# Optimization experiments

Hardware: AMD Instinct MI355X
Metric: run time of the kernel (lower is better)

Reference implementation:

```python
import jax, jax.numpy as jnp
import numpy as np

B, S, D, H = 2, 2048, 1024, 16
DK = D // H

def setup_inputs() -> dict:
    key = jax.random.key(0)
    ks = jax.random.split(key, 12)
    s = 1.0 / np.sqrt(D)
    inp = {
        'q': jax.random.normal(ks[0], (B, S, D), jnp.float32),
        'k': jax.random.normal(ks[1], (B, S, D), jnp.float32),
        'v': jax.random.normal(ks[2], (B, S, D), jnp.float32),
        'mask': jnp.tril(jnp.ones((S, S), jnp.int32))[None, None],  # [1,1,S,S] causal
        'Wq': jax.random.normal(ks[3], (D, D), jnp.float32) * s,
        'bq': jax.random.normal(ks[4], (D,), jnp.float32) * s,
        'Wk': jax.random.normal(ks[5], (D, D), jnp.float32) * s,
        'bk': jax.random.normal(ks[6], (D,), jnp.float32) * s,
        'Wv': jax.random.normal(ks[7], (D, D), jnp.float32) * s,
        'bv': jax.random.normal(ks[8], (D,), jnp.float32) * s,
        'Wo': jax.random.normal(ks[9], (D, D), jnp.float32) * s,
        'bo': jax.random.normal(ks[10], (D,), jnp.float32) * s,
    }
    return inp

def reference(q, k, v, mask, Wq, bq, Wk, bk, Wv, bv, Wo, bo):
    # linear projections (torch nn.Linear: x @ W.T + b)
    query = q @ Wq.T + bq
    key_ = k @ Wk.T + bk
    value = v @ Wv.T + bv
    # [B,S,D] -> [B,H,S,dk]
    def split_heads(x):
        return x.reshape(B, S, H, DK).transpose(0, 2, 1, 3)
    query, key_, value = split_heads(query), split_heads(key_), split_heads(value)
    scores = jnp.einsum('bhqd,bhkd->bhqk', query, key_) / jnp.sqrt(jnp.float32(DK))
    scores = jnp.where(mask == 0, jnp.float32(-1e9), scores)
    # FAITHFUL to source: softmax over dim=1 (the HEAD axis), not dim=-1
    attn = jax.nn.softmax(scores, axis=1)
    x = jnp.einsum('bhqk,bhkd->bhqd', attn, value)
    x = x.transpose(0, 2, 1, 3).reshape(B, S, D)
    return x @ Wo.T + bo
```

## Files before the change

kernel.cpp:

```cpp
#include <hip/hip_runtime.h>
#include <hip/hip_bf16.h>
#include <stdint.h>
#include <stddef.h>


typedef __attribute__((ext_vector_type(8))) __bf16 bf16x8;
typedef __attribute__((ext_vector_type(4))) __bf16 bf16x4;
typedef __attribute__((ext_vector_type(2))) _Float16 f16x2;
typedef __attribute__((ext_vector_type(4))) _Float16 f16x4;
typedef __attribute__((ext_vector_type(8))) _Float16 f16x8;
typedef __attribute__((ext_vector_type(4))) float  f32x4;
typedef __attribute__((ext_vector_type(8))) float  f32x8;

#define MFMA_BF16_K32(a,b,c) __builtin_amdgcn_mfma_f32_16x16x32_bf16((a),(b),(c),0,0,0)
#define MFMA_F16_K16(a,b,c)  __builtin_amdgcn_mfma_f32_16x16x16f16((a),(b),(c),0,0,0)

template <typename T> __device__ inline f32x8 ld8(const T* p);
template <> __device__ inline f32x8 ld8<float>(const float* p) { return *(const f32x8*)p; }
template <> __device__ inline f32x8 ld8<__bf16>(const __bf16* p) {
  return __builtin_convertvector(*(const bf16x8*)p, f32x8);
}

__device__ __forceinline__ void gl_lds16(const __bf16* g, __bf16* l) {
  __builtin_amdgcn_global_load_lds(
      (const __attribute__((address_space(1))) void*)g,
      (__attribute__((address_space(3))) void*)l, 16, 0, 0);
}

__device__ __forceinline__ f16x2 pk2(float a, float b) {
  return __builtin_bit_cast(f16x2, __builtin_amdgcn_cvt_pkrtz(a, b));
}

__device__ __forceinline__ void epi_store(int mode, float val, int m, int n, void* dst) {
  if (mode == 0) {
    ((float*)dst)[(size_t)m * 1024 + n] = val;
  } else if (mode == 2) {
    const int bb = m >> 11, s = m & 2047, h = n >> 6, dhi = (n >> 5) & 1, dlo = n & 31;
    ((__bf16*)dst)[(size_t)((h * 2 + dhi) * 2 + bb) * 65536 + s * 32 + dlo] = (__bf16)val;
  } else {
    const int bb = m >> 11, s = m & 2047, h = n >> 6, d = n & 63;
    ((_Float16*)dst)[((((size_t)bb * 128 + (s >> 4)) * 16 + h) * 64 + d) * 16 + (s & 15)] =
        (_Float16)val;
  }
}

struct CvtArgs { const float* src[7]; __bf16* dst[7]; };

__global__ __launch_bounds__(256) void cvt_kernel(CvtArgs a, int nqkv, int nw) {
  const int t = blockIdx.y;
  const int n = (t < 3) ? nqkv : nw;
  const int base = (blockIdx.x * 256 + threadIdx.x) * 8;
  if (base >= n) return;
  *(bf16x8*)(a.dst[t] + base) =
      __builtin_convertvector(*(const f32x8*)(a.src[t] + base), bf16x8);
}

struct GemmSet {
  const __bf16* A0[3]; const __bf16* A1[3]; const __bf16* A2[3]; const __bf16* A3[3];
  const __bf16* W[3]; const float* bias[3]; void* dst[3]; int mode[3];
};

__global__ __launch_bounds__(256) void gemm_tile(GemmSet g) {
  const int z = blockIdx.z;
  const __bf16* __restrict__ A0 = g.A0[z];
  const __bf16* __restrict__ A1 = g.A1[z];
  const __bf16* __restrict__ A2 = g.A2[z];
  const __bf16* __restrict__ A3 = g.A3[z];
  const __bf16* __restrict__ W  = g.W[z];
  const float*  __restrict__ bias = g.bias[z];
  void* dst = g.dst[z];
  const int mode = g.mode[z];

  __shared__ __bf16 As[128 * 64];
  __shared__ __bf16 Bs[128 * 64];
  const int tid  = threadIdx.x;
  const int lane = tid & 63, wid = tid >> 6;
  const int l15  = lane & 15, quad = lane >> 4;
  const int m0   = blockIdx.y * 128;
  const int n0   = blockIdx.x * 128;
  const int srow = lane >> 3;
  const int swz  = ((lane & 7) ^ srow) * 8;
  const int wm   = (wid >> 1) * 64;
  const int wn   = (wid & 1) * 64;
  const int mr = tid >> 3;
  const int mc = tid & 7;
  const int mg = ((mc ^ (mr & 7)) * 8);

  f32x4 acc[4][4] = {};

  for (int k0 = 0; k0 < 1024; k0 += 64) {
    if (A1 != nullptr) {
      #pragma unroll
      for (int gI = 0; gI < 4; ++gI) {
        const size_t gi = (size_t)(m0 + gI * 32 + mr) * 1024 + k0 + mg;
        f32x8 s = ld8(&A0[gi]) + ld8(&A1[gi]) + ld8(&A2[gi]) + ld8(&A3[gi]);
        *(bf16x8*)&As[(gI * 32 + mr) * 64 + mc * 8] = __builtin_convertvector(s, bf16x8);
      }
    } else {
      #pragma unroll
      for (int i = 0; i < 4; ++i)
        gl_lds16(A0 + (size_t)(m0 + wid * 32 + i * 8 + srow) * 1024 + k0 + swz,
                 &As[(wid * 32 + i * 8) * 64]);
    }
    #pragma unroll
    for (int i = 0; i < 4; ++i)
      gl_lds16(W + (size_t)(n0 + wid * 32 + i * 8 + srow) * 1024 + k0 + swz,
               &Bs[(wid * 32 + i * 8) * 64]);
    __syncthreads();
    #pragma unroll
    for (int kk = 0; kk < 64; kk += 32) {
      const int slot = (((kk >> 3) + quad) ^ (l15 & 7)) * 8;
      bf16x8 fa[4], fb[4];
      #pragma unroll
      for (int ms = 0; ms < 4; ++ms)
        fa[ms] = *(const bf16x8*)&As[(wm + ms * 16 + l15) * 64 + slot];
      #pragma unroll
      for (int ns = 0; ns < 4; ++ns)
        fb[ns] = *(const bf16x8*)&Bs[(wn + ns * 16 + l15) * 64 + slot];
      #pragma unroll
      for (int ms = 0; ms < 4; ++ms)
        #pragma unroll
        for (int ns = 0; ns < 4; ++ns)
          acc[ms][ns] = MFMA_BF16_K32(fa[ms], fb[ns], acc[ms][ns]);
    }
    __syncthreads();
  }

  #pragma unroll
  for (int ms = 0; ms < 4; ++ms) {
    #pragma unroll
    for (int ns = 0; ns < 4; ++ns) {
      const int n     = n0 + wn + ns * 16 + l15;
      const float bv  = bias[n];
      const int mbase = m0 + wm + ms * 16 + quad * 4;
      #pragma unroll
      for (int r = 0; r < 4; ++r)
        epi_store(mode, acc[ms][ns][r] + bv, mbase + r, n, dst);
    }
  }
}

template <typename TA>
__global__ __launch_bounds__(256) void gemm_bt(
    const TA* __restrict__ A0, const TA* __restrict__ A1,
    const float* __restrict__ W, const float* __restrict__ bias,
    void* dst, int mode)
{
  __shared__ __bf16 As[64][72];
  __shared__ __bf16 Bs[64][72];
  const int tid  = threadIdx.x;
  const int m0   = blockIdx.y * 64;
  const int n0   = blockIdx.x * 64;
  const int row  = tid >> 3;
  const int seg  = (tid & 7) * 8;
  const int lane = tid & 63;
  const int wid  = tid >> 6;
  const int l15  = lane & 15;
  const int quad = lane >> 4;
  const int wm   = (wid >> 1) * 32;
  const int wn   = (wid & 1) * 32;

  f32x4 acc[2][2] = {};

  for (int k0 = 0; k0 < 1024; k0 += 64) {
    const size_t i0 = (size_t)(m0 + row) * 1024 + k0 + seg;
    const size_t i1 = (size_t)(m0 + row + 32) * 1024 + k0 + seg;
    f32x8 a0 = ld8(&A0[i0]);
    f32x8 a1 = ld8(&A0[i1]);
    if (A1) { a0 += ld8(&A1[i0]); a1 += ld8(&A1[i1]); }
    f32x8 b0 = ld8(&W[(size_t)(n0 + row) * 1024 + k0 + seg]);
    f32x8 b1 = ld8(&W[(size_t)(n0 + row + 32) * 1024 + k0 + seg]);
    *(bf16x8*)&As[row][seg]      = __builtin_convertvector(a0, bf16x8);
    *(bf16x8*)&As[row + 32][seg] = __builtin_convertvector(a1, bf16x8);
    *(bf16x8*)&Bs[row][seg]      = __builtin_convertvector(b0, bf16x8);
    *(bf16x8*)&Bs[row + 32][seg] = __builtin_convertvector(b1, bf16x8);
    __syncthreads();
    #pragma unroll
    for (int kk = 0; kk < 64; kk += 32) {
      bf16x8 fa0 = *(const bf16x8*)&As[wm + l15][kk + quad * 8];
      bf16x8 fa1 = *(const bf16x8*)&As[wm + 16 + l15][kk + quad * 8];
      bf16x8 fb0 = *(const bf16x8*)&Bs[wn + l15][kk + quad * 8];
      bf16x8 fb1 = *(const bf16x8*)&Bs[wn + 16 + l15][kk + quad * 8];
      acc[0][0] = MFMA_BF16_K32(fa0, fb0, acc[0][0]);
      acc[0][1] = MFMA_BF16_K32(fa0, fb1, acc[0][1]);
      acc[1][0] = MFMA_BF16_K32(fa1, fb0, acc[1][0]);
      acc[1][1] = MFMA_BF16_K32(fa1, fb1, acc[1][1]);
    }
    __syncthreads();
  }

  #pragma unroll
  for (int ms = 0; ms < 2; ++ms) {
    #pragma unroll
    for (int ns = 0; ns < 2; ++ns) {
      const int n     = n0 + wn + ns * 16 + l15;
      const float bv  = bias[n];
      const int mbase = m0 + wm + ms * 16 + quad * 4;
      #pragma unroll
      for (int r = 0; r < 4; ++r)
        epi_store(mode, acc[ms][ns][r] + bv, mbase + r, n, dst);
    }
  }
}

__global__ __launch_bounds__(256) void tilesum_kernel(
    const _Float16* __restrict__ Vl, float* __restrict__ tsum)
{
  const int gid = blockIdx.x * 256 + threadIdx.x;
  const _Float16* p = Vl + (size_t)gid * 16;
  f32x8 s = __builtin_convertvector(*(const f16x8*)p, f32x8) +
            __builtin_convertvector(*(const f16x8*)(p + 8), f32x8);
  float tot = 0.f;
  #pragma unroll
  for (int i = 0; i < 8; ++i) tot += s[i];
  tsum[gid] = tot;
}

__global__ __launch_bounds__(64) void scan_kernel(
    const float* __restrict__ tsum, float* __restrict__ suffix)
{
  const int gid = blockIdx.x * 64 + threadIdx.x;
  const int hd = gid & 1023;
  const int b  = gid >> 10;
  const float* tp = tsum + (size_t)b * 131072 + hd;
  float* sp = suffix + (size_t)b * 131072 + hd;
  float run = 0.f;
  #pragma unroll 4
  for (int kt = 127; kt >= 0; --kt) {
    sp[(size_t)kt * 1024] = run * 0.0625f;
    run += tp[(size_t)kt * 1024];
  }
}

__global__ __launch_bounds__(256) void sufscan_kernel(
    const _Float16* __restrict__ Vl, float* __restrict__ suffix)
{
  const int gid = blockIdx.x * 256 + threadIdx.x;
  const int hd = gid & 1023;
  const int b  = gid >> 10;
  float run = 0.f;
  for (int kt = 127; kt >= 0; --kt) {
    suffix[((size_t)(b * 128 + kt)) * 1024 + hd] = run * 0.0625f;
    const _Float16* p = Vl + ((size_t)(b * 128 + kt) * 1024 + hd) * 16;
    f32x8 s = __builtin_convertvector(*(const f16x8*)p, f32x8) +
              __builtin_convertvector(*(const f16x8*)(p + 8), f32x8);
    float tot = 0.f;
    #pragma unroll
    for (int i = 0; i < 8; ++i) tot += s[i];
    run += tot;
  }
}

__global__ __launch_bounds__(256, 2) void attn_kernel(
    const __bf16* __restrict__ Qs, const __bf16* __restrict__ Ks,
    const _Float16* __restrict__ Vl, const float* __restrict__ suffix,
    __bf16* __restrict__ P0, __bf16* __restrict__ P1,
    __bf16* __restrict__ P2, __bf16* __restrict__ P3, int lnsl)
{
  __shared__ float Pf[2][2][4][16][20];

  const int tid   = threadIdx.x;
  const int nsl   = 1 << lnsl;
  const int slice = blockIdx.x & (nsl - 1);
  const int rest  = blockIdx.x >> lnsl;
  const int b     = rest & 1;
  const int t     = 127 - (rest >> 1);
  const int q0    = t * 16;
  const int nt    = t + 1;
  const int tbeg  = (slice * nt) >> lnsl;
  const int tend  = ((slice + 1) * nt) >> lnsl;

  const int lane = tid & 63, wid = tid >> 6;
  const int l15 = lane & 15, quad = lane >> 4;
  const float kSc = 0.18033688011112042f;

  bf16x8 qf[4][2];
  #pragma unroll
  for (int hh = 0; hh < 4; ++hh) {
    const int h = wid * 4 + hh;
    #pragma unroll
    for (int dhi = 0; dhi < 2; ++dhi)
      qf[hh][dhi] = *(const bf16x8*)&Qs[(size_t)((h * 2 + dhi) * 2 + b) * 65536
                                        + (q0 + l15) * 32 + quad * 8];
  }

  f32x4 acc[4][4] = {};
  int buf = 0;

  bf16x8 kf[4][2][2];
  auto load_k = [&](int ct) {
    const int cc1 = (ct + 1 < 128) ? ct + 1 : 127;
    const int ccl[2] = {ct, cc1};
    #pragma unroll
    for (int hh = 0; hh < 4; ++hh) {
      const int h = wid * 4 + hh;
      #pragma unroll
      for (int j = 0; j < 2; ++j) {
        const int krow = ccl[j] * 16 + l15;
        #pragma unroll
        for (int dhi = 0; dhi < 2; ++dhi)
          kf[hh][j][dhi] = *(const bf16x8*)&Ks[(size_t)((h * 2 + dhi) * 2 + b) * 65536
                                                + krow * 32 + quad * 8];
      }
    }
  };
  if (tbeg < tend) load_k(tbeg);

  for (int ct = tbeg; ct < tend; ct += 2, buf ^= 1) {
    const int ntc = (tend - ct) < 2 ? 1 : 2;
    const int cc1 = (ct + 1 < 128) ? ct + 1 : 127;
    const int ccl[2] = {ct, cc1};

    float e[4][2][4];
    float ps[2][4] = {};
    #pragma unroll
    for (int hh = 0; hh < 4; ++hh) {
      #pragma unroll
      for (int j = 0; j < 2; ++j) {
        f32x4 s = {};
        s = MFMA_BF16_K32(kf[hh][j][0], qf[hh][0], s);
        s = MFMA_BF16_K32(kf[hh][j][1], qf[hh][1], s);
        const bool dg = (ccl[j] == t);
        #pragma unroll
        for (int r = 0; r < 4; ++r) {
          float x = s[r] * kSc;
          if (dg) x = (quad * 4 + r > l15) ? 0.f : x;
          float ev = exp2f(x);
          if (j >= ntc) ev = 0.f;
          e[hh][j][r] = ev;
          ps[j][r] += ev;
        }
      }
    }
    #pragma unroll
    for (int j = 0; j < 2; ++j) {
      f32x4 v; v[0] = ps[j][0]; v[1] = ps[j][1]; v[2] = ps[j][2]; v[3] = ps[j][3];
      *(f32x4*)&Pf[buf][j][wid][l15][quad * 4] = v;
    }

    f16x4 vf[4][2][4];
    #pragma unroll
    for (int hh = 0; hh < 4; ++hh) {
      const int h = wid * 4 + hh;
      #pragma unroll
      for (int j = 0; j < 2; ++j) {
        const _Float16* vb = Vl + ((size_t)(b * 128 + ccl[j]) * 16 + h) * 1024;
        #pragma unroll
        for (int n = 0; n < 4; ++n)
          vf[hh][j][n] = *(const f16x4*)(vb + (n * 16 + l15) * 16 + quad * 4);
      }
    }

    if (ct + 2 < tend) load_k(ct + 2);

    __syncthreads();

    float inv[2][4];
    #pragma unroll
    for (int j = 0; j < 2; ++j) {
      f32x4 tot = *(const f32x4*)&Pf[buf][j][0][l15][quad * 4];
      #pragma unroll
      for (int w = 1; w < 4; ++w)
        tot += *(const f32x4*)&Pf[buf][j][w][l15][quad * 4];
      #pragma unroll
      for (int r = 0; r < 4; ++r)
        inv[j][r] = __builtin_amdgcn_rcpf(fmaxf(tot[r], 1e-30f));
    }

    #pragma unroll
    for (int hh = 0; hh < 4; ++hh) {
      #pragma unroll
      for (int j = 0; j < 2; ++j) {
        if (j >= ntc) break;
        f16x2 lo = pk2(e[hh][j][0] * inv[j][0], e[hh][j][1] * inv[j][1]);
        f16x2 hi = pk2(e[hh][j][2] * inv[j][2], e[hh][j][3] * inv[j][3]);
        f16x4 af = __builtin_shufflevector(lo, hi, 0, 1, 2, 3);
        #pragma unroll
        for (int n = 0; n < 4; ++n)
          acc[hh][n] = MFMA_F16_K16(af, vf[hh][j][n], acc[hh][n]);
      }
    }
  }

  __bf16* Pout = slice == 0 ? P0 : slice == 1 ? P1 : slice == 2 ? P2 : P3;
  const bool last = (slice == nsl - 1);
  #pragma unroll
  for (int hh = 0; hh < 4; ++hh) {
    const int h = wid * 4 + hh;
    #pragma unroll
    for (int n = 0; n < 4; ++n) {
      const float sfx =
          last ? suffix[((size_t)(b * 128 + t)) * 1024 + h * 64 + n * 16 + l15] : 0.f;
      #pragma unroll
      for (int r = 0; r < 4; ++r)
        Pout[((size_t)(b * 2048 + q0 + quad * 4 + r)) * 1024 + h * 64 + n * 16 + l15] =
            (__bf16)(acc[hh][n][r] + sfx);
    }
  }
}

extern "C" void kernel_launch(void* const* d_in, const int* in_sizes, int n_in,
                              void* d_out, int out_size, void* d_ws, size_t ws_size,
                              hipStream_t stream) {
  const float* q  = (const float*)d_in[0];
  const float* k  = (const float*)d_in[1];
  const float* v  = (const float*)d_in[2];
  const float* Wq = (const float*)d_in[4];
  const float* bq = (const float*)d_in[5];
  const float* Wk = (const float*)d_in[6];
  const float* bk = (const float*)d_in[7];
  const float* Wv = (const float*)d_in[8];
  const float* bv = (const float*)d_in[9];
  const float* Wo = (const float*)d_in[10];
  const float* bo = (const float*)d_in[11];

  char* ws = (char*)d_ws;
  const size_t MiB = 1ull << 20;

  if (ws_size >= 67 * MiB) {
    __bf16* qc  = (__bf16*)(ws +  0 * MiB);
    __bf16* kc  = (__bf16*)(ws +  8 * MiB);
    __bf16* vc  = (__bf16*)(ws + 16 * MiB);
    __bf16* Wqc = (__bf16*)(ws + 24 * MiB);
    __bf16* Wkc = (__bf16*)(ws + 26 * MiB);
    __bf16* Wvc = (__bf16*)(ws + 28 * MiB);
    __bf16* Woc = (__bf16*)(ws + 30 * MiB);
    __bf16* Qs  = (__bf16*)(ws + 32 * MiB);
    __bf16* Ks  = (__bf16*)(ws + 40 * MiB);
    _Float16* Vl = (_Float16*)(ws + 48 * MiB);
    __bf16* P0  = (__bf16*)(ws + 56 * MiB);
    float* suffix = (float*)(ws + 64 * MiB);
    float* tsum   = (float*)(ws + 65 * MiB);

    CvtArgs ca;
    ca.src[0] = q;  ca.dst[0] = qc;
    ca.src[1] = k;  ca.dst[1] = kc;
    ca.src[2] = v;  ca.dst[2] = vc;
    ca.src[3] = Wq; ca.dst[3] = Wqc;
    ca.src[4] = Wk; ca.dst[4] = Wkc;
    ca.src[5] = Wv; ca.dst[5] = Wvc;
    ca.src[6] = Wo; ca.dst[6] = Woc;
    cvt_kernel<<<dim3(2048, 7), 256, 0, stream>>>(ca, 4194304, 1048576);

    GemmSet g3 = {};
    g3.A0[0] = qc; g3.W[0] = Wqc; g3.bias[0] = bq; g3.dst[0] = Qs; g3.mode[0] = 2;
    g3.A0[1] = kc; g3.W[1] = Wkc; g3.bias[1] = bk; g3.dst[1] = Ks; g3.mode[1] = 2;
    g3.A0[2] = vc; g3.W[2] = Wvc; g3.bias[2] = bv; g3.dst[2] = Vl; g3.mode[2] = 3;
    gemm_tile<<<dim3(8, 32, 3), 256, 0, stream>>>(g3);

    tilesum_kernel<<<1024, 256, 0, stream>>>(Vl, tsum);
    scan_kernel<<<32, 64, 0, stream>>>(tsum, suffix);
    attn_kernel<<<1024, 256, 0, stream>>>(Qs, Ks, Vl, suffix, P0, qc, kc, vc, 2);

    GemmSet go = {};
    go.A0[0] = P0; go.A1[0] = qc; go.A2[0] = kc; go.A3[0] = vc;
    go.W[0] = Woc; go.bias[0] = bo; go.dst[0] = d_out; go.mode[0] = 0;
    gemm_tile<<<dim3(8, 32, 1), 256, 0, stream>>>(go);
  } else {
    __bf16* Qs  = (__bf16*)(ws);
    __bf16* Ks  = (__bf16*)(ws +  8 * MiB);
    _Float16* Vl = (_Float16*)(ws + 16 * MiB);
    __bf16* P0  = (__bf16*)(ws + 24 * MiB);
    __bf16* P1  = (__bf16*)(ws + 32 * MiB);
    float* suffix = (float*)(ws + 40 * MiB);

    dim3 gg(16, 64, 1);
    gemm_bt<float><<<gg, 256, 0, stream>>>(q, nullptr, Wq, bq, Qs, 2);
    gemm_bt<float><<<gg, 256, 0, stream>>>(k, nullptr, Wk, bk, Ks, 2);
    gemm_bt<float><<<gg, 256, 0, stream>>>(v, nullptr, Wv, bv, Vl, 3);
    sufscan_kernel<<<8, 256, 0, stream>>>(Vl, suffix);
    attn_kernel<<<512, 256, 0, stream>>>(Qs, Ks, Vl, suffix, P0, P1, P1, P1, 1);
    gemm_bt<__bf16><<<gg, 256, 0, stream>>>(P0, P1, Wo, bo, d_out, 0);
  }
}
```

Baseline: 357.3 us.

## Process two query tiles per block with 8 waves and 2 heads per wave

The attention kernel now uses 512-thread blocks that each handle a pair of query tiles, with 8 waves each owning 2 heads instead of 4 waves owning 4 heads. Each K and V fragment load now serves two query tiles, which halves K/V global traffic per query and halves the grid size. The K prefetch across iterations is removed, and the softmax numerators are packed to fp16 and scaled with fp16 multiplies. The risks are less overlap of K loads, a larger LDS reduction across 8 waves, and a coarser grid that may balance the causal workload less evenly.

```diff
diff --git a/kernel.cpp b/kernel.cpp
--- a/kernel.cpp
+++ b/kernel.cpp
@@ -251,97 +251,108 @@
   }
 }
 
-__global__ __launch_bounds__(256, 2) void attn_kernel(
+__global__ __launch_bounds__(512, 2) void attn_kernel(
     const __bf16* __restrict__ Qs, const __bf16* __restrict__ Ks,
     const _Float16* __restrict__ Vl, const float* __restrict__ suffix,
     __bf16* __restrict__ P0, __bf16* __restrict__ P1,
     __bf16* __restrict__ P2, __bf16* __restrict__ P3, int lnsl)
 {
-  __shared__ float Pf[2][2][4][16][20];
-
-  const int tid   = threadIdx.x;
+  __shared__ float Pf[2][2][2][8][256];
+
   const int nsl   = 1 << lnsl;
-  const int slice = blockIdx.x & (nsl - 1);
-  const int rest  = blockIdx.x >> lnsl;
-  const int b     = rest & 1;
-  const int t     = 127 - (rest >> 1);
-  const int q0    = t * 16;
-  const int nt    = t + 1;
+  const int rank  = blockIdx.x;
+  const int jpt   = 2 * nsl;
+  const int tp    = 63 - rank / jpt;
+  const int sub   = rank % jpt;
+  const int b     = sub & 1;
+  const int slice = sub >> 1;
+  const int t0    = 2 * tp, t1 = 2 * tp + 1;
+  const int nt    = t1 + 1;
   const int tbeg  = (slice * nt) >> lnsl;
   const int tend  = ((slice + 1) * nt) >> lnsl;
 
+  const int tid  = threadIdx.x;
   const int lane = tid & 63, wid = tid >> 6;
-  const int l15 = lane & 15, quad = lane >> 4;
+  const int l15  = lane & 15, quad = lane >> 4;
   const float kSc = 0.18033688011112042f;
 
-  bf16x8 qf[4][2];
+  bf16x8 qf[2][2][2];
   #pragma unroll
-  for (int hh = 0; hh < 4; ++hh) {
-    const int h = wid * 4 + hh;
-    #pragma unroll
-    for (int dhi = 0; dhi < 2; ++dhi)
-      qf[hh][dhi] = *(const bf16x8*)&Qs[(size_t)((h * 2 + dhi) * 2 + b) * 65536
-                                        + (q0 + l15) * 32 + quad * 8];
-  }
-
-  f32x4 acc[4][4] = {};
+  for (int hh = 0; hh < 2; ++hh) {
+    const int h = wid * 2 + hh;
+    #pragma unroll
+    for (int qs = 0; qs < 2; ++qs)
+      #pragma unroll
+      for (int dhi = 0; dhi < 2; ++dhi)
+        qf[hh][qs][dhi] = *(const bf16x8*)&Qs[(size_t)((h * 2 + dhi) * 2 + b) * 65536
+                                              + ((t0 + qs) * 16 + l15) * 32 + quad * 8];
+  }
+
+  f32x4 acc[2][2][4] = {};
   int buf = 0;
-
-  bf16x8 kf[4][2][2];
-  auto load_k = [&](int ct) {
-    const int cc1 = (ct + 1 < 128) ? ct + 1 : 127;
-    const int ccl[2] = {ct, cc1};
-    #pragma unroll
-    for (int hh = 0; hh < 4; ++hh) {
-      const int h = wid * 4 + hh;
-      #pragma unroll
-      for (int j = 0; j < 2; ++j) {
-        const int krow = ccl[j] * 16 + l15;
-        #pragma unroll
-        for (int dhi = 0; dhi < 2; ++dhi)
-          kf[hh][j][dhi] = *(const bf16x8*)&Ks[(size_t)((h * 2 + dhi) * 2 + b) * 65536
-                                                + krow * 32 + quad * 8];
-      }
-    }
-  };
-  if (tbeg < tend) load_k(tbeg);
 
   for (int ct = tbeg; ct < tend; ct += 2, buf ^= 1) {
     const int ntc = (tend - ct) < 2 ? 1 : 2;
     const int cc1 = (ct + 1 < 128) ? ct + 1 : 127;
     const int ccl[2] = {ct, cc1};
 
-    float e[4][2][4];
-    float ps[2][4] = {};
-    #pragma unroll
-    for (int hh = 0; hh < 4; ++hh) {
+    bf16x8 kf[2][2][2];
+    #pragma unroll
+    for (int hh = 0; hh < 2; ++hh) {
+      const int h = wid * 2 + hh;
       #pragma unroll
       for (int j = 0; j < 2; ++j) {
-        f32x4 s = {};
-        s = MFMA_BF16_K32(kf[hh][j][0], qf[hh][0], s);
-        s = MFMA_BF16_K32(kf[hh][j][1], qf[hh][1], s);
-        const bool dg = (ccl[j] == t);
-        #pragma unroll
-        for (int r = 0; r < 4; ++r) {
-          float x = s[r] * kSc;
-          if (dg) x = (quad * 4 + r > l15) ? 0.f : x;
-          float ev = exp2f(x);
-          if (j >= ntc) ev = 0.f;
-          e[hh][j][r] = ev;
-          ps[j][r] += ev;
+        const int krow = ccl[j] * 16 + l15;
+        #pragma unroll
+        for (int dhi = 0; dhi < 2; ++dhi)
+          kf[hh][j][dhi] = *(const bf16x8*)&Ks[(size_t)((h * 2 + dhi) * 2 + b) * 65536
+                                                + krow * 32 + quad * 8];
+      }
+    }
+
+    f16x2 eh[2][2][2][2];
+    float ps[2][2][4] = {};
+    #pragma unroll
+    for (int hh = 0; hh < 2; ++hh) {
+      #pragma unroll
+      for (int j = 0; j < 2; ++j) {
+        #pragma unroll
+        for (int qs = 0; qs < 2; ++qs) {
+          f32x4 s = {};
+          s = MFMA_BF16_K32(kf[hh][j][0], qf[hh][qs][0], s);
+          s = MFMA_BF16_K32(kf[hh][j][1], qf[hh][qs][1], s);
+          const int qt = t0 + qs;
+          const bool full = (ccl[j] > qt) || (j >= ntc);
+          const bool diag = (ccl[j] == qt);
+          float ev[4];
+          #pragma unroll
+          for (int r = 0; r < 4; ++r) {
+            if (full) { ev[r] = 0.f; }
+            else {
+              float xv = s[r] * kSc;
+              if (diag) xv = (quad * 4 + r > l15) ? 0.f : xv;
+              ev[r] = exp2f(xv);
+            }
+            ps[j][qs][r] += ev[r];
+          }
+          eh[hh][j][qs][0] = pk2(ev[0], ev[1]);
+          eh[hh][j][qs][1] = pk2(ev[2], ev[3]);
         }
       }
     }
     #pragma unroll
-    for (int j = 0; j < 2; ++j) {
-      f32x4 v; v[0] = ps[j][0]; v[1] = ps[j][1]; v[2] = ps[j][2]; v[3] = ps[j][3];
-      *(f32x4*)&Pf[buf][j][wid][l15][quad * 4] = v;
-    }
-
-    f16x4 vf[4][2][4];
-    #pragma unroll
-    for (int hh = 0; hh < 4; ++hh) {
-      const int h = wid * 4 + hh;
+    for (int j = 0; j < 2; ++j)
+      #pragma unroll
+      for (int qs = 0; qs < 2; ++qs) {
+        f32x4 v; v[0] = ps[j][qs][0]; v[1] = ps[j][qs][1];
+        v[2] = ps[j][qs][2]; v[3] = ps[j][qs][3];
+        *(f32x4*)&Pf[buf][j][qs][wid][l15 * 16 + quad * 4] = v;
+      }
+
+    f16x4 vf[2][2][4];
+    #pragma unroll
+    for (int hh = 0; hh < 2; ++hh) {
+      const int h = wid * 2 + hh;
       #pragma unroll
       for (int j = 0; j < 2; ++j) {
         const _Float16* vb = Vl + ((size_t)(b * 128 + ccl[j]) * 16 + h) * 1024;
@@ -350,34 +361,41 @@
           vf[hh][j][n] = *(const f16x4*)(vb + (n * 16 + l15) * 16 + quad * 4);
       }
     }
-
-    if (ct + 2 < tend) load_k(ct + 2);
-
     __syncthreads();
 
-    float inv[2][4];
+    f16x2 invh[2][2][2];
     #pragma unroll
     for (int j = 0; j < 2; ++j) {
-      f32x4 tot = *(const f32x4*)&Pf[buf][j][0][l15][quad * 4];
-      #pragma unroll
-      for (int w = 1; w < 4; ++w)
-        tot += *(const f32x4*)&Pf[buf][j][w][l15][quad * 4];
-      #pragma unroll
-      for (int r = 0; r < 4; ++r)
-        inv[j][r] = __builtin_amdgcn_rcpf(fmaxf(tot[r], 1e-30f));
-    }
-
-    #pragma unroll
-    for (int hh = 0; hh < 4; ++hh) {
+      #pragma unroll
+      for (int qs = 0; qs < 2; ++qs) {
+        f32x4 tot = *(const f32x4*)&Pf[buf][j][qs][0][l15 * 16 + quad * 4];
+        #pragma unroll
+        for (int w = 1; w < 8; ++w)
+          tot += *(const f32x4*)&Pf[buf][j][qs][w][l15 * 16 + quad * 4];
+        float iv[4];
+        #pragma unroll
+        for (int r = 0; r < 4; ++r)
+          iv[r] = __builtin_amdgcn_rcpf(fmaxf(tot[r], 1e-30f));
+        invh[j][qs][0] = pk2(iv[0], iv[1]);
+        invh[j][qs][1] = pk2(iv[2], iv[3]);
+      }
+    }
+
+    #pragma unroll
+    for (int hh = 0; hh < 2; ++hh) {
       #pragma unroll
       for (int j = 0; j < 2; ++j) {
         if (j >= ntc) break;
-        f16x2 lo = pk2(e[hh][j][0] * inv[j][0], e[hh][j][1] * inv[j][1]);
-        f16x2 hi = pk2(e[hh][j][2] * inv[j][2], e[hh][j][3] * inv[j][3]);
-        f16x4 af = __builtin_shufflevector(lo, hi, 0, 1, 2, 3);
-        #pragma unroll
-        for (int n = 0; n < 4; ++n)
-          acc[hh][n] = MFMA_F16_K16(af, vf[hh][j][n], acc[hh][n]);
+        #pragma unroll
+        for (int qs = 0; qs < 2; ++qs) {
+          if (ccl[j] > t0 + qs) continue;
+          f16x2 lo = eh[hh][j][qs][0] * invh[j][qs][0];
+          f16x2 hi = eh[hh][j][qs][1] * invh[j][qs][1];
+          f16x4 af = __builtin_shufflevector(lo, hi, 0, 1, 2, 3);
+          #pragma unroll
+          for (int n = 0; n < 4; ++n)
+            acc[hh][qs][n] = MFMA_F16_K16(af, vf[hh][j][n], acc[hh][qs][n]);
+        }
       }
     }
   }
@@ -385,16 +403,20 @@
   __bf16* Pout = slice == 0 ? P0 : slice == 1 ? P1 : slice == 2 ? P2 : P3;
   const bool last = (slice == nsl - 1);
   #pragma unroll
-  for (int hh = 0; hh < 4; ++hh) {
-    const int h = wid * 4 + hh;
-    #pragma unroll
-    for (int n = 0; n < 4; ++n) {
-      const float sfx =
-          last ? suffix[((size_t)(b * 128 + t)) * 1024 + h * 64 + n * 16 + l15] : 0.f;
-      #pragma unroll
-      for (int r = 0; r < 4; ++r)
-        Pout[((size_t)(b * 2048 + q0 + quad * 4 + r)) * 1024 + h * 64 + n * 16 + l15] =
-            (__bf16)(acc[hh][n][r] + sfx);
+  for (int hh = 0; hh < 2; ++hh) {
+    const int h = wid * 2 + hh;
+    #pragma unroll
+    for (int qs = 0; qs < 2; ++qs) {
+      const int t = t0 + qs;
+      #pragma unroll
+      for (int n = 0; n < 4; ++n) {
+        const float sfx =
+            last ? suffix[((size_t)(b * 128 + t)) * 1024 + h * 64 + n * 16 + l15] : 0.f;
+        #pragma unroll
+        for (int r = 0; r < 4; ++r)
+          Pout[((size_t)(b * 2048 + t * 16 + quad * 4 + r)) * 1024 + h * 64 + n * 16 + l15] =
+              (__bf16)(acc[hh][qs][n][r] + sfx);
+      }
     }
   }
 }
@@ -450,7 +472,7 @@
 
     tilesum_kernel<<<1024, 256, 0, stream>>>(Vl, tsum);
     scan_kernel<<<32, 64, 0, stream>>>(tsum, suffix);
-    attn_kernel<<<1024, 256, 0, stream>>>(Qs, Ks, Vl, suffix, P0, qc, kc, vc, 2);
+    attn_kernel<<<512, 512, 0, stream>>>(Qs, Ks, Vl, suffix, P0, qc, kc, vc, 2);
 
     GemmSet go = {};
     go.A0[0] = P0; go.A1[0] = qc; go.A2[0] = kc; go.A3[0] = vc;
@@ -469,7 +491,7 @@
     gemm_bt<float><<<gg, 256, 0, stream>>>(k, nullptr, Wk, bk, Ks, 2);
     gemm_bt<float><<<gg, 256, 0, stream>>>(v, nullptr, Wv, bv, Vl, 3);
     sufscan_kernel<<<8, 256, 0, stream>>>(Vl, suffix);
-    attn_kernel<<<512, 256, 0, stream>>>(Qs, Ks, Vl, suffix, P0, P1, P1, P1, 1);
+    attn_kernel<<<256, 512, 0, stream>>>(Qs, Ks, Vl, suffix, P0, P1, P1, P1, 1);
     gemm_bt<__bf16><<<gg, 256, 0, stream>>>(P0, P1, Wo, bo, d_out, 0);
   }
 }
```

Result: slower. 443.7 us (+24.2%).
